# Optimization experiments

Measured on AMD Instinct MI355X. Metric: run time of the kernel, lower is better.

The kernel has to match this reference:

```python
import jax, jax.numpy as jnp
import numpy as np

B, S, D_EMBED, D_HIDDEN = 4, 256, 300, 300
C = 5.0  # frozen tanh-scaling constant


def setup_inputs() -> dict:
    key = jax.random.key(0)
    ks = jax.random.split(key, 8)
    w = 0.05  # ~xavier scale for 300x300
    return {
        "inputs": jax.random.normal(ks[0], (B, S, D_EMBED), jnp.float32),
        "rep_mask": jax.random.randint(ks[1], (B, S), 0, 2, jnp.int32),
        "W_fc": jax.random.normal(ks[2], (D_HIDDEN, D_EMBED), jnp.float32) * w,
        "b_fc": jnp.zeros((D_HIDDEN,), jnp.float32),
        "W1": jax.random.normal(ks[3], (D_HIDDEN, D_HIDDEN), jnp.float32) * w,
        "W2": jax.random.normal(ks[4], (D_HIDDEN, D_HIDDEN), jnp.float32) * w,
        "b1": jnp.zeros((D_HIDDEN,), jnp.float32),
        "W_f1": jax.random.normal(ks[5], (D_HIDDEN, D_HIDDEN), jnp.float32) * w,
        "W_f2": jax.random.normal(ks[6], (D_HIDDEN, D_HIDDEN), jnp.float32) * w,
        "b_f": jnp.zeros((D_HIDDEN,), jnp.float32),
    }


def _disa_fwd(inputs, rep_mask_f, W_fc, b_fc, W1, W2, b1, W_f1, W_f2, b_f):
    n_seq = inputs.shape[1]
    # forward direction mask: attend to strictly later positions (triu, diag=1)
    direct = jnp.triu(jnp.ones((n_seq, n_seq), inputs.dtype), k=1)
    # mask[b,i,j] = rep_mask[b,j] * direct[i,j], shape [B,S,S,1]
    mask = (rep_mask_f[:, None, :] * direct[None]) [..., None]

    rep_map = jax.nn.elu(jnp.einsum('bse,he->bsh', inputs, W_fc) + b_fc)  # [B,S,D]
    dep = jnp.einsum('bsh,gh->bsg', rep_map, W1)   # dependent (token j)
    head = jnp.einsum('bsh,gh->bsg', rep_map, W2)  # head (token i)

    # logits[b,i,j,d]
    logits = C * jnp.tanh((dep[:, None, :, :] + head[:, :, None, :] + b1) / C)

    # hand-rolled masked softmax over dim=2 (j), faithful to original
    masked = logits * mask
    mx = jnp.max(masked, axis=2, keepdims=True)
    exps = jnp.exp(masked - mx) * mask
    sums = jnp.sum(exps, axis=2, keepdims=True)
    sums = sums + (sums == 0).astype(logits.dtype)
    attn = (exps / (sums + 1e-20)) * mask

    attn_result = jnp.sum(attn * rep_map[:, None, :, :], axis=2)  # [B,S,D]

    gate = jax.nn.sigmoid(
        jnp.einsum('bsh,gh->bsg', rep_map, W_f1)
        + jnp.einsum('bsh,gh->bsg', attn_result, W_f2)
        + b_f
    )
    out = gate * rep_map + (1.0 - gate) * attn_result
    return out * rep_mask_f[..., None]


def reference(inputs, rep_mask, W_fc, b_fc, W1, W2, b1, W_f1, W_f2, b_f):
    rep_mask_f = rep_mask.astype(inputs.dtype)
    return _disa_fwd(inputs, rep_mask_f, W_fc, b_fc, W1, W2, b1, W_f1, W_f2, b_f)
```

## Files before the change

kernel.cpp:

```cpp
#include <hip/hip_runtime.h>
#include <hip/hip_bf16.h>

#define Dx 300
#define Mx 1024

#define OFF_REP    0
#define OFF_DEP    307200
#define OFF_HEAD   614400
#define OFF_ATTN   921600
#define U_BASE     1228800
#define REPB       0
#define ATB        327680

typedef __attribute__((ext_vector_type(8))) short short8;
typedef __attribute__((ext_vector_type(4))) float f32x4;

union S8 { unsigned int u[4]; unsigned short s[8]; short8 v; };

__device__ __forceinline__ float bf2f(unsigned short u) {
    union { unsigned int i; float f; } v; v.i = ((unsigned int)u) << 16; return v.f;
}
__device__ __forceinline__ unsigned short f2bf(float x) {
    union { float f; unsigned int i; } u; u.f = x;
    return (unsigned short)((u.i + 0x8000u) >> 16);
}
__device__ __forceinline__ int detect_bf16(const void* w) {
    const unsigned short* u = (const unsigned short*)w;
    int ok = 1;
    #pragma unroll
    for (int t = 0; t < 64; ++t) { float v = bf2f(u[t]); ok &= (fabsf(v) < 1.0f) ? 1 : 0; }
    return ok;
}
__device__ __forceinline__ float ldf(const void* p, int idx, int isbf) {
    return isbf ? bf2f(((const unsigned short*)p)[idx]) : ((const float*)p)[idx];
}

__device__ __forceinline__ void load8f(const float* rowp, int kb, int kmax,
                                       int valid, float* x) {
    if (valid && kb + 8 <= kmax) {
        float4 a = *(const float4*)(rowp + kb);
        float4 b = *(const float4*)(rowp + kb + 4);
        x[0]=a.x; x[1]=a.y; x[2]=a.z; x[3]=a.w;
        x[4]=b.x; x[5]=b.y; x[6]=b.z; x[7]=b.w;
    } else {
        #pragma unroll
        for (int j = 0; j < 8; ++j) {
            int k = kb + j;
            x[j] = (valid && k < kmax) ? rowp[k] : 0.f;
        }
    }
}
__device__ __forceinline__ short8 pack8(const float* x) {
    S8 H;
    #pragma unroll
    for (int p = 0; p < 4; ++p) {
        union { float f; unsigned int i; } a, b;
        a.f = x[2*p]; b.f = x[2*p+1];
        H.u[p] = ((a.i + 0x8000u) >> 16) | ((b.i + 0x8000u) & 0xFFFF0000u);
    }
    return H.v;
}
__device__ __forceinline__ short8 load8bf(const unsigned short* rowp, int kb,
                                          int kmax, int valid) {
    S8 R;
    if (valid && kb + 8 <= kmax) {
        ushort4 a = *(const ushort4*)(rowp + kb);
        ushort4 b = *(const ushort4*)(rowp + kb + 4);
        R.s[0]=a.x; R.s[1]=a.y; R.s[2]=a.z; R.s[3]=a.w;
        R.s[4]=b.x; R.s[5]=b.y; R.s[6]=b.z; R.s[7]=b.w;
    } else {
        #pragma unroll
        for (int j = 0; j < 8; ++j) {
            int k = kb + j;
            R.s[j] = (valid && k < kmax) ? rowp[k] : (unsigned short)0;
        }
    }
    return R.v;
}
__device__ __forceinline__ short8 loadB(const void* W, int row, int kb, int isbf,
                                        int valid) {
    if (isbf) return load8bf((const unsigned short*)W + row * 300, kb, 300, valid);
    float t[8];
    load8f((const float*)W + row * 300, kb, 300, valid, t);
    return pack8(t);
}

__global__ __launch_bounds__(256) void k_mm1(
        const void* __restrict__ Xv, const void* __restrict__ Wfc,
        const void* __restrict__ bfc, float* __restrict__ ws) {
    __shared__ int s_isbf;
    if (threadIdx.x == 0) s_isbf = detect_bf16(Wfc);
    __syncthreads();
    const int isbf = s_isbf;
    const int tid = threadIdx.x, w = tid >> 6, l = tid & 63;
    const int mt = blockIdx.x / 5, nt = blockIdx.x % 5;
    const int m0 = mt * 16, lm = l & 15, koff = (l >> 4) * 8;
    const int nrow = nt * 64 + w * 16 + lm;
    const int bval = nrow < 300;
    const int ncl = bval ? nrow : 0;
    unsigned short* U = (unsigned short*)(ws + U_BASE);
    f32x4 acc = {0.f, 0.f, 0.f, 0.f};
    if (isbf) {
        const unsigned short* Xp = (const unsigned short*)Xv + (m0 + lm) * 300;
        #pragma unroll
        for (int ks = 0; ks < 10; ++ks) {
            short8 a = load8bf(Xp, ks*32 + koff, 300, 1);
            short8 b = loadB(Wfc, ncl, ks*32 + koff, 1, bval);
            acc = __builtin_amdgcn_mfma_f32_16x16x32_bf16(a, b, acc, 0, 0, 0);
        }
    } else {
        const float* Xp = (const float*)Xv + (m0 + lm) * 300;
        #pragma unroll
        for (int ks = 0; ks < 10; ++ks) {
            float t[8]; load8f(Xp, ks*32 + koff, 300, 1, t);
            short8 a = pack8(t);
            short8 b = loadB(Wfc, ncl, ks*32 + koff, 0, bval);
            acc = __builtin_amdgcn_mfma_f32_16x16x32_bf16(a, b, acc, 0, 0, 0);
        }
    }
    if (bval) {
        float bb = ldf(bfc, nrow, isbf);
        #pragma unroll
        for (int r = 0; r < 4; ++r) {
            int mg = m0 + (l >> 4) * 4 + r;
            float v = acc[r] + bb;
            v = v > 0.f ? v : (__expf(v) - 1.f);
            ws[OFF_REP + mg * 300 + nrow] = v;
            U[REPB + mg * 320 + nrow] = f2bf(v);
        }
    } else {
        #pragma unroll
        for (int r = 0; r < 4; ++r) {
            int mg = m0 + (l >> 4) * 4 + r;
            U[REPB + mg * 320 + nrow] = 0;
        }
    }
}

__global__ __launch_bounds__(256) void k_mm2(
        const void* __restrict__ W1, const void* __restrict__ W2,
        const void* __restrict__ b1, float* __restrict__ ws) {
    __shared__ int s_isbf;
    if (threadIdx.x == 0) s_isbf = detect_bf16(W1);
    __syncthreads();
    const int isbf = s_isbf;
    const int tid = threadIdx.x, w = tid >> 6, l = tid & 63;
    const int mt = blockIdx.x / 10, nt = blockIdx.x % 10;
    const int m0 = mt * 16, lm = l & 15, koff = (l >> 4) * 8;
    const int ng = nt * 64 + w * 16 + lm;
    const int wsel = ng < 320;
    const int wrow = wsel ? ng : ng - 320;
    const int bval = wrow < 300;
    const int wcl = bval ? wrow : 0;
    const void* Wp = wsel ? W1 : W2;
    const unsigned short* U = (const unsigned short*)(ws + U_BASE);
    const unsigned short* ap = U + REPB + (m0 + lm) * 320 + koff;
    f32x4 acc = {0.f, 0.f, 0.f, 0.f};
    #pragma unroll
    for (int ks = 0; ks < 10; ++ks) {
        short8 a = *(const short8*)(ap + ks * 32);
        short8 b = loadB(Wp, wcl, ks*32 + koff, isbf, bval);
        acc = __builtin_amdgcn_mfma_f32_16x16x32_bf16(a, b, acc, 0, 0, 0);
    }
    if (ng < 300) {
        float bb = ldf(b1, ng, isbf);
        #pragma unroll
        for (int r = 0; r < 4; ++r) {
            int mg = m0 + (l >> 4) * 4 + r;
            ws[OFF_DEP + mg * 300 + ng] = __expf(0.4f * (acc[r] + bb));
        }
    } else if (ng >= 320 && ng < 620) {
        #pragma unroll
        for (int r = 0; r < 4; ++r) {
            int mg = m0 + (l >> 4) * 4 + r;
            ws[OFF_HEAD + mg * 300 + (ng - 320)] = acc[r];
        }
    }
}

__global__ __launch_bounds__(320) void k_attn(
        float* __restrict__ ws, const int* __restrict__ mask) {
    const float* exd  = ws + OFF_DEP;
    const float* head = ws + OFF_HEAD;
    const float* rep  = ws + OFF_REP;
    unsigned short* U = (unsigned short*)(ws + U_BASE);
    __shared__ float mkf[256];
    const int blk = blockIdx.x;
    const int b = blk >> 7;
    const int tile = blk & 127;
    const int u = tile >> 1;
    const int i0 = (tile & 1) ? (254 - 2 * u) : (2 * u);
    const int tid = threadIdx.x;
    if (tid < 256) mkf[tid] = (float)mask[b * 256 + tid];
    __syncthreads();
    const int d = tid;
    const int base = b * 256;
    if (d >= 300) {
        U[ATB + (base + i0) * 320 + d] = 0;
        U[ATB + (base + i0 + 1) * 320 + d] = 0;
        return;
    }

    const float hv0 = head[(base + i0) * Dx + d];
    const float hv1 = head[(base + i0 + 1) * Dx + d];
    const float pw0 = __expf(0.4f * hv0);
    const float pw1 = __expf(0.4f * hv1);

    float s0 = 0.f, r0 = 0.f, s1 = 0.f, r1 = 0.f;
    {
        const int j = i0 + 1;
        float ex = exd[(base + j) * Dx + d];
        float rv = rep[(base + j) * Dx + d];
        float mk = mkf[j];
        float u0 = fmaf(ex, pw0, 1.0f);
        float e0 = __expf(-10.0f * __builtin_amdgcn_rcpf(u0));
        float em0 = e0 * mk;
        s0 += em0; r0 = fmaf(em0, rv, r0);
    }
    const float* ep = exd + base * Dx + d;
    const float* rp = rep + base * Dx + d;
    #pragma unroll 4
    for (int j = i0 + 2; j < 256; ++j) {
        float ex = ep[j * Dx];
        float rv = rp[j * Dx];
        float mk = mkf[j];
        float u0 = fmaf(ex, pw0, 1.0f);
        float u1 = fmaf(ex, pw1, 1.0f);
        float e0 = __expf(-10.0f * __builtin_amdgcn_rcpf(u0));
        float e1 = __expf(-10.0f * __builtin_amdgcn_rcpf(u1));
        float em0 = e0 * mk;
        float em1 = e1 * mk;
        s0 += em0; r0 = fmaf(em0, rv, r0);
        s1 += em1; r1 = fmaf(em1, rv, r1);
    }
    const float den0 = s0 + (s0 == 0.f ? 1.f : 0.f) + 1e-20f;
    const float den1 = s1 + (s1 == 0.f ? 1.f : 0.f) + 1e-20f;
    const float a0 = r0 / den0, a1 = r1 / den1;
    ws[OFF_ATTN + (base + i0) * Dx + d]     = a0;
    ws[OFF_ATTN + (base + i0 + 1) * Dx + d] = a1;
    U[ATB + (base + i0) * 320 + d]     = f2bf(a0);
    U[ATB + (base + i0 + 1) * 320 + d] = f2bf(a1);
}

__global__ __launch_bounds__(256) void k_mm3(
        const void* __restrict__ Wf1, const void* __restrict__ Wf2,
        const void* __restrict__ bfv, const int* __restrict__ mask,
        float* __restrict__ ws, void* __restrict__ outv) {
    __shared__ int s_isbf;
    if (threadIdx.x == 0) s_isbf = detect_bf16(Wf1);
    __syncthreads();
    const int isbf = s_isbf;
    const int tid = threadIdx.x, w = tid >> 6, l = tid & 63;
    const int mt = blockIdx.x / 5, nt = blockIdx.x % 5;
    const int m0 = mt * 16, lm = l & 15, koff = (l >> 4) * 8;
    const int nrow = nt * 64 + w * 16 + lm;
    const int bval = nrow < 300;
    const int ncl = bval ? nrow : 0;
    const unsigned short* U = (const unsigned short*)(ws + U_BASE);
    const unsigned short* a1p = U + REPB + (m0 + lm) * 320 + koff;
    const unsigned short* a2p = U + ATB  + (m0 + lm) * 320 + koff;
    f32x4 acc = {0.f, 0.f, 0.f, 0.f};
    #pragma unroll
    for (int ks = 0; ks < 10; ++ks) {
        short8 a = *(const short8*)(a1p + ks * 32);
        short8 b = loadB(Wf1, ncl, ks*32 + koff, isbf, bval);
        acc = __builtin_amdgcn_mfma_f32_16x16x32_bf16(a, b, acc, 0, 0, 0);
    }
    #pragma unroll
    for (int ks = 0; ks < 10; ++ks) {
        short8 a = *(const short8*)(a2p + ks * 32);
        short8 b = loadB(Wf2, ncl, ks*32 + koff, isbf, bval);
        acc = __builtin_amdgcn_mfma_f32_16x16x32_bf16(a, b, acc, 0, 0, 0);
    }
    if (bval) {
        float bb = ldf(bfv, nrow, isbf);
        #pragma unroll
        for (int r = 0; r < 4; ++r) {
            int mg = m0 + (l >> 4) * 4 + r;
            float gp = acc[r] + bb;
            float gate = 1.0f / (1.0f + __expf(-gp));
            float rv = ws[OFF_REP  + mg * 300 + nrow];
            float av = ws[OFF_ATTN + mg * 300 + nrow];
            float res = (gate * rv + (1.0f - gate) * av) * (float)mask[mg];
            if (isbf) ((__hip_bfloat16*)outv)[mg * 300 + nrow] = __float2bfloat16(res);
            else      ((float*)outv)[mg * 300 + nrow] = res;
        }
    }
}

extern "C" void kernel_launch(void* const* d_in, const int* in_sizes, int n_in,
                              void* d_out, int out_size, void* d_ws, size_t ws_size,
                              hipStream_t stream) {
    const void* X   = d_in[0];
    const int*  msk = (const int*)d_in[1];
    const void* Wfc = d_in[2];
    const void* bfc = d_in[3];
    const void* W1  = d_in[4];
    const void* W2  = d_in[5];
    const void* b1  = d_in[6];
    const void* Wf1 = d_in[7];
    const void* Wf2 = d_in[8];
    const void* bfv = d_in[9];
    float* ws = (float*)d_ws;

    hipLaunchKernelGGL(k_mm1,  dim3(320), dim3(256), 0, stream, X, Wfc, bfc, ws);
    hipLaunchKernelGGL(k_mm2,  dim3(640), dim3(256), 0, stream, W1, W2, b1, ws);
    hipLaunchKernelGGL(k_attn, dim3(512), dim3(320), 0, stream, ws, msk);
    hipLaunchKernelGGL(k_mm3,  dim3(320), dim3(256), 0, stream,
                       Wf1, Wf2, bfv, msk, ws, d_out);
}
```

Measured before the change: 137.4 us.

## Fuse first projection and W1/W2 projections into one kernel via shared memory

```diff
diff --git a/kernel.cpp b/kernel.cpp
--- a/kernel.cpp
+++ b/kernel.cpp
@@ -85,95 +85,108 @@
     return pack8(t);
 }
 
-__global__ __launch_bounds__(256) void k_mm1(
+__global__ __launch_bounds__(640) void k_head(
         const void* __restrict__ Xv, const void* __restrict__ Wfc,
-        const void* __restrict__ bfc, float* __restrict__ ws) {
+        const void* __restrict__ bfc, const void* __restrict__ W1,
+        const void* __restrict__ W2,  const void* __restrict__ b1,
+        float* __restrict__ ws) {
+    __shared__ __align__(16) unsigned short repL[16][328];
     __shared__ int s_isbf;
-    if (threadIdx.x == 0) s_isbf = detect_bf16(Wfc);
+    const int tid = threadIdx.x;
+    if (tid == 0) s_isbf = detect_bf16(Wfc);
+    if (tid < 448) {
+        int m = tid / 28, c = 300 + tid % 28;
+        repL[m][c] = 0;
+    }
     __syncthreads();
     const int isbf = s_isbf;
-    const int tid = threadIdx.x, w = tid >> 6, l = tid & 63;
-    const int mt = blockIdx.x / 5, nt = blockIdx.x % 5;
-    const int m0 = mt * 16, lm = l & 15, koff = (l >> 4) * 8;
-    const int nrow = nt * 64 + w * 16 + lm;
-    const int bval = nrow < 300;
-    const int ncl = bval ? nrow : 0;
+    const int w = tid >> 6, l = tid & 63;
+    const int lm = l & 15, koff = (l >> 4) * 8;
+    const int mt = blockIdx.x >> 1, half = blockIdx.x & 1;
+    const int m0 = mt * 16;
     unsigned short* U = (unsigned short*)(ws + U_BASE);
-    f32x4 acc = {0.f, 0.f, 0.f, 0.f};
+
+    short8 xa[10];
     if (isbf) {
         const unsigned short* Xp = (const unsigned short*)Xv + (m0 + lm) * 300;
         #pragma unroll
-        for (int ks = 0; ks < 10; ++ks) {
-            short8 a = load8bf(Xp, ks*32 + koff, 300, 1);
-            short8 b = loadB(Wfc, ncl, ks*32 + koff, 1, bval);
-            acc = __builtin_amdgcn_mfma_f32_16x16x32_bf16(a, b, acc, 0, 0, 0);
-        }
+        for (int ks = 0; ks < 10; ++ks) xa[ks] = load8bf(Xp, ks*32 + koff, 300, 1);
     } else {
         const float* Xp = (const float*)Xv + (m0 + lm) * 300;
         #pragma unroll
         for (int ks = 0; ks < 10; ++ks) {
             float t[8]; load8f(Xp, ks*32 + koff, 300, 1, t);
-            short8 a = pack8(t);
-            short8 b = loadB(Wfc, ncl, ks*32 + koff, 0, bval);
-            acc = __builtin_amdgcn_mfma_f32_16x16x32_bf16(a, b, acc, 0, 0, 0);
-        }
-    }
-    if (bval) {
-        float bb = ldf(bfc, nrow, isbf);
-        #pragma unroll
-        for (int r = 0; r < 4; ++r) {
-            int mg = m0 + (l >> 4) * 4 + r;
-            float v = acc[r] + bb;
-            v = v > 0.f ? v : (__expf(v) - 1.f);
-            ws[OFF_REP + mg * 300 + nrow] = v;
-            U[REPB + mg * 320 + nrow] = f2bf(v);
-        }
-    } else {
-        #pragma unroll
-        for (int r = 0; r < 4; ++r) {
-            int mg = m0 + (l >> 4) * 4 + r;
-            U[REPB + mg * 320 + nrow] = 0;
-        }
-    }
-}
-
-__global__ __launch_bounds__(256) void k_mm2(
-        const void* __restrict__ W1, const void* __restrict__ W2,
-        const void* __restrict__ b1, float* __restrict__ ws) {
-    __shared__ int s_isbf;
-    if (threadIdx.x == 0) s_isbf = detect_bf16(W1);
+            xa[ks] = pack8(t);
+        }
+    }
+    #pragma unroll
+    for (int s = 0; s < 2; ++s) {
+        const int ns = w + s * 10;
+        if (ns < 19) {
+            const int nb = ns * 16 + lm;
+            const int bval = nb < 300;
+            const int ncl = bval ? nb : 0;
+            f32x4 acc = {0.f, 0.f, 0.f, 0.f};
+            #pragma unroll
+            for (int ks = 0; ks < 10; ++ks) {
+                short8 b = loadB(Wfc, ncl, ks*32 + koff, isbf, bval);
+                acc = __builtin_amdgcn_mfma_f32_16x16x32_bf16(xa[ks], b, acc, 0, 0, 0);
+            }
+            if (bval) {
+                float bb = ldf(bfc, nb, isbf);
+                #pragma unroll
+                for (int r = 0; r < 4; ++r) {
+                    int ml = (l >> 4) * 4 + r;
+                    float v = acc[r] + bb;
+                    v = v > 0.f ? v : (__expf(v) - 1.f);
+                    unsigned short hv = f2bf(v);
+                    repL[ml][nb] = hv;
+                    if (half == 0) {
+                        ws[OFF_REP + (m0 + ml) * 300 + nb] = v;
+                        U[REPB + (m0 + ml) * 320 + nb] = hv;
+                    }
+                }
+            }
+        }
+    }
+    if (half == 0 && tid < 320) {
+        int m = tid / 20, c = 300 + tid % 20;
+        U[REPB + (m0 + m) * 320 + c] = 0;
+    }
     __syncthreads();
-    const int isbf = s_isbf;
-    const int tid = threadIdx.x, w = tid >> 6, l = tid & 63;
-    const int mt = blockIdx.x / 10, nt = blockIdx.x % 10;
-    const int m0 = mt * 16, lm = l & 15, koff = (l >> 4) * 8;
-    const int ng = nt * 64 + w * 16 + lm;
-    const int wsel = ng < 320;
-    const int wrow = wsel ? ng : ng - 320;
-    const int bval = wrow < 300;
-    const int wcl = bval ? wrow : 0;
-    const void* Wp = wsel ? W1 : W2;
-    const unsigned short* U = (const unsigned short*)(ws + U_BASE);
-    const unsigned short* ap = U + REPB + (m0 + lm) * 320 + koff;
-    f32x4 acc = {0.f, 0.f, 0.f, 0.f};
-    #pragma unroll
-    for (int ks = 0; ks < 10; ++ks) {
-        short8 a = *(const short8*)(ap + ks * 32);
-        short8 b = loadB(Wp, wcl, ks*32 + koff, isbf, bval);
-        acc = __builtin_amdgcn_mfma_f32_16x16x32_bf16(a, b, acc, 0, 0, 0);
-    }
-    if (ng < 300) {
-        float bb = ldf(b1, ng, isbf);
-        #pragma unroll
-        for (int r = 0; r < 4; ++r) {
-            int mg = m0 + (l >> 4) * 4 + r;
-            ws[OFF_DEP + mg * 300 + ng] = __expf(0.4f * (acc[r] + bb));
-        }
-    } else if (ng >= 320 && ng < 620) {
-        #pragma unroll
-        for (int r = 0; r < 4; ++r) {
-            int mg = m0 + (l >> 4) * 4 + r;
-            ws[OFF_HEAD + mg * 300 + (ng - 320)] = acc[r];
+
+    short8 ra[10];
+    #pragma unroll
+    for (int ks = 0; ks < 10; ++ks)
+        ra[ks] = *(const short8*)&repL[lm][ks*32 + koff];
+    #pragma unroll
+    for (int s = 0; s < 2; ++s) {
+        const int ns2 = w + s * 10 + half * 20;
+        const int ng = ns2 * 16 + lm;
+        const int wsel = ng < 320;
+        const int wrow = wsel ? ng : ng - 320;
+        const int bval = wrow < 300;
+        const int wcl = bval ? wrow : 0;
+        const void* Wp = wsel ? W1 : W2;
+        f32x4 acc = {0.f, 0.f, 0.f, 0.f};
+        #pragma unroll
+        for (int ks = 0; ks < 10; ++ks) {
+            short8 b = loadB(Wp, wcl, ks*32 + koff, isbf, bval);
+            acc = __builtin_amdgcn_mfma_f32_16x16x32_bf16(ra[ks], b, acc, 0, 0, 0);
+        }
+        if (ng < 300) {
+            float bb = ldf(b1, ng, isbf);
+            #pragma unroll
+            for (int r = 0; r < 4; ++r) {
+                int mg = m0 + (l >> 4) * 4 + r;
+                ws[OFF_DEP + mg * 300 + ng] = __expf(0.4f * (acc[r] + bb));
+            }
+        } else if (ng >= 320 && ng < 620) {
+            #pragma unroll
+            for (int r = 0; r < 4; ++r) {
+                int mg = m0 + (l >> 4) * 4 + r;
+                ws[OFF_HEAD + mg * 300 + (ng - 320)] = acc[r];
+            }
         }
     }
 }
@@ -303,8 +316,8 @@
     const void* bfv = d_in[9];
     float* ws = (float*)d_ws;
 
-    hipLaunchKernelGGL(k_mm1,  dim3(320), dim3(256), 0, stream, X, Wfc, bfc, ws);
-    hipLaunchKernelGGL(k_mm2,  dim3(640), dim3(256), 0, stream, W1, W2, b1, ws);
+    hipLaunchKernelGGL(k_head, dim3(128), dim3(640), 0, stream,
+                       X, Wfc, bfc, W1, W2, b1, ws);
     hipLaunchKernelGGL(k_attn, dim3(512), dim3(320), 0, stream, ws, msk);
     hipLaunchKernelGGL(k_mm3,  dim3(320), dim3(256), 0, stream,
                        Wf1, Wf2, bfv, msk, ws, d_out);
```

New measurement: 144.8 us. 1.05x slower.
